# Optimization experiments

Hardware: AMD Instinct MI355X
Metric: run time of the kernel (lower is better)

## Reference

```python
import jax, jax.numpy as jnp
import numpy as np


def setup_inputs() -> dict:
    key = jax.random.key(0)
    k1, k2, k3 = jax.random.split(key, 3)
    B, N, L, H, E = 4, 4, 1024, 8, 64
    queries = jax.random.normal(k1, (B, N, L, H, E), dtype=jnp.float32)
    keys = jax.random.normal(k2, (B, N, L, H, E), dtype=jnp.float32)
    values = jax.random.normal(k3, (B, N, L, H, E), dtype=jnp.float32)
    return {"queries": queries, "keys": keys, "values": values}


def reference(queries, keys, values):
    B, N, L, H, E = queries.shape
    S = values.shape[2]
    scale = 1.0 / jnp.sqrt(jnp.asarray(E, queries.dtype))
    # scores: [B, N, H, L, S]
    scores = jnp.einsum('bnlhe,bnshe->bnhls', queries, keys)
    # causal mask: True above the diagonal (future positions), broadcast over b,n,h
    causal = jnp.triu(jnp.ones((L, S), dtype=bool), k=1)
    scores = jnp.where(causal, -jnp.inf, scores)
    A = jax.nn.softmax(scale * scores, axis=-1)  # dropout p=0.0 -> identity
    V = jnp.einsum('bnhls,bnshd->bnlhd', A, values)
    return V
```

## Files before the change

kernel.cpp:

```cpp
#include <hip/hip_runtime.h>
#include <hip/hip_bf16.h>


typedef __bf16 bf16x8 __attribute__((ext_vector_type(8)));
typedef float  f32x16 __attribute__((ext_vector_type(16)));
typedef unsigned int u32x4 __attribute__((ext_vector_type(4)));

#define SEQ 1024
#define ROWSTRIDE 512
#define LDSPAD 72

__device__ inline bf16x8 pack8(float4 a, float4 b) {
    bf16x8 f;
    f[0]=(__bf16)a.x; f[1]=(__bf16)a.y; f[2]=(__bf16)a.z; f[3]=(__bf16)a.w;
    f[4]=(__bf16)b.x; f[5]=(__bf16)b.y; f[6]=(__bf16)b.z; f[7]=(__bf16)b.w;
    return f;
}
__device__ inline bf16x8 pack8s(float4 a, float4 b, float s) {
    bf16x8 f;
    f[0]=(__bf16)(a.x*s); f[1]=(__bf16)(a.y*s); f[2]=(__bf16)(a.z*s); f[3]=(__bf16)(a.w*s);
    f[4]=(__bf16)(b.x*s); f[5]=(__bf16)(b.y*s); f[6]=(__bf16)(b.z*s); f[7]=(__bf16)(b.w*s);
    return f;
}
__device__ inline unsigned int packbf2(float a, float b) {
    unsigned short ua = __builtin_bit_cast(unsigned short, (__bf16)a);
    unsigned short ub = __builtin_bit_cast(unsigned short, (__bf16)b);
    return (unsigned int)ua | ((unsigned int)ub << 16);
}

__device__ inline void lds_barrier() {
    asm volatile("s_waitcnt lgkmcnt(0)\n\ts_barrier" ::: "memory");
}

__global__ __launch_bounds__(256) void attn_fwd(
    const float* __restrict__ Qg,
    const float* __restrict__ Kg,
    const float* __restrict__ Vg,
    float* __restrict__ Og)
{
    __shared__ __bf16 Kds[64][LDSPAD];
    __shared__ __bf16 Vds[64][LDSPAD];

    const int blk  = blockIdx.x;
    const int t    = blk >> 7;
    const int head = blk & 127;
    const int h_   = head & 7;
    const int bn   = head >> 3;
    const int qt0  = 2 * t, qt1 = 2 * t + 1;

    const int tid  = threadIdx.x;
    const int wave = tid >> 6;
    const int lane = tid & 63;
    const int hh   = lane >> 5;
    const int l31  = lane & 31;
    const int l15  = lane & 15;
    const int state = l31 >> 4;

    const size_t base = (size_t)bn * SEQ * ROWSTRIDE + (size_t)h_ * 64;

    const int qt_lane   = state ? qt1 : qt0;
    const int q_in_tile = wave * 16 + l15;
    const int qrow_lane = qt_lane * 64 + q_in_tile;

    const float kscale = 0.125f * 1.44269504088896f;

    bf16x8 qf[4];
    {
        const float* qp = Qg + base + (size_t)qrow_lane * ROWSTRIDE + 8 * hh;
        #pragma unroll
        for (int ks = 0; ks < 4; ++ks)
            qf[ks] = pack8s(*(const float4*)(qp + 16 * ks),
                            *(const float4*)(qp + 16 * ks + 4), kscale);
    }

    f32x16 o[2];
    #pragma unroll
    for (int et = 0; et < 2; ++et)
        #pragma unroll
        for (int i = 0; i < 16; ++i) o[et][i] = 0.f;
    float lsum = 0.f;

    const int sr = tid >> 2, sc = (tid & 3) << 4;
    const int ve = tid & 63, vs = (tid >> 6) << 4;

    const int ntiles = qt1 + 1;
    const float* kbase = Kg + base;
    const float* vbase = Vg + base;

    float4 kpre[4];
    float  vpre[16];
    {
        const float* kp = kbase + (size_t)sr * ROWSTRIDE + sc;
        #pragma unroll
        for (int i = 0; i < 4; ++i) kpre[i] = *(const float4*)(kp + i * 4);
        const float* vp = vbase + (size_t)vs * ROWSTRIDE + ve;
        #pragma unroll
        for (int j = 0; j < 16; ++j) vpre[j] = vp[(size_t)j * ROWSTRIDE];
    }

    for (int tile = 0; tile < ntiles; ++tile) {
        lds_barrier();

        *(bf16x8*)&Kds[sr][sc]     = pack8(kpre[0], kpre[1]);
        *(bf16x8*)&Kds[sr][sc + 8] = pack8(kpre[2], kpre[3]);
        {
            bf16x8 f0, f1;
            #pragma unroll
            for (int jj = 0; jj < 8; ++jj) { f0[jj] = (__bf16)vpre[jj]; f1[jj] = (__bf16)vpre[8 + jj]; }
            *(bf16x8*)&Vds[ve][vs]     = f0;
            *(bf16x8*)&Vds[ve][vs + 8] = f1;
        }

        if (tile + 1 < ntiles) {
            const int s0n = (tile + 1) * 64;
            const float* kp = kbase + (size_t)(s0n + sr) * ROWSTRIDE + sc;
            #pragma unroll
            for (int i = 0; i < 4; ++i) kpre[i] = *(const float4*)(kp + i * 4);
            const float* vp = vbase + (size_t)(s0n + vs) * ROWSTRIDE + ve;
            #pragma unroll
            for (int j = 0; j < 16; ++j) vpre[j] = vp[(size_t)j * ROWSTRIDE];
        }

        lds_barrier();

        const bool masked = (tile >= qt0);
        const int slimit = !masked ? 64
                         : ((tile < qt_lane) ? 64
                         : ((tile == qt_lane) ? q_in_tile : -1));

        #pragma unroll
        for (int st2 = 0; st2 < 2; ++st2) {
            f32x16 s16;
            #pragma unroll
            for (int i = 0; i < 16; ++i) s16[i] = 0.f;
            #pragma unroll
            for (int ks = 0; ks < 4; ++ks) {
                bf16x8 kb = *(const bf16x8*)&Kds[st2 * 32 + l31][ks * 16 + 8 * hh];
                s16 = __builtin_amdgcn_mfma_f32_32x32x16_bf16(kb, qf[ks], s16, 0, 0, 0);
            }
            unsigned int Dp[8];
            float ps[16];
            if (!masked) {
                #pragma unroll
                for (int reg = 0; reg < 16; ++reg) {
                    float p = __builtin_amdgcn_exp2f(s16[reg]);
                    lsum += p;
                    ps[reg] = p;
                }
            } else {
                #pragma unroll
                for (int reg = 0; reg < 16; ++reg) {
                    const int s_in = st2 * 32 + (reg & 3) + 8 * (reg >> 2) + 4 * hh;
                    float p = (s_in <= slimit) ? __builtin_amdgcn_exp2f(s16[reg]) : 0.f;
                    lsum += p;
                    ps[reg] = p;
                }
            }
            #pragma unroll
            for (int i = 0; i < 8; ++i) Dp[i] = packbf2(ps[2 * i], ps[2 * i + 1]);

            #pragma unroll
            for (int kh = 0; kh < 2; ++kh) {
                const int ks = st2 * 2 + kh;
                const int ka = 4 * kh;
                unsigned int own0 = hh ? Dp[ka + 2] : Dp[ka + 0];
                unsigned int own1 = hh ? Dp[ka + 3] : Dp[ka + 1];
                unsigned int snd0 = hh ? Dp[ka + 0] : Dp[ka + 2];
                unsigned int snd1 = hh ? Dp[ka + 1] : Dp[ka + 3];
                unsigned int x0 = (unsigned int)__shfl_xor((int)snd0, 32);
                unsigned int x1 = (unsigned int)__shfl_xor((int)snd1, 32);
                u32x4 g;
                g[0] = hh ? x0 : own0;
                g[1] = hh ? x1 : own1;
                g[2] = hh ? own0 : x0;
                g[3] = hh ? own1 : x1;
                bf16x8 pf = __builtin_bit_cast(bf16x8, g);
                #pragma unroll
                for (int et = 0; et < 2; ++et) {
                    bf16x8 vb = *(const bf16x8*)&Vds[et * 32 + l31][ks * 16 + 8 * hh];
                    o[et] = __builtin_amdgcn_mfma_f32_32x32x16_bf16(vb, pf, o[et], 0, 0, 0);
                }
            }
        }
    }

    lsum += __shfl_xor(lsum, 32);
    const float inv_l = 1.f / lsum;
    float* op = Og + base + (size_t)qrow_lane * ROWSTRIDE + 4 * hh;
    #pragma unroll
    for (int et = 0; et < 2; ++et) {
        #pragma unroll
        for (int g = 0; g < 4; ++g) {
            float4 v;
            v.x = o[et][4 * g + 0] * inv_l;
            v.y = o[et][4 * g + 1] * inv_l;
            v.z = o[et][4 * g + 2] * inv_l;
            v.w = o[et][4 * g + 3] * inv_l;
            *(float4*)(op + et * 32 + g * 8) = v;
        }
    }
}

extern "C" void kernel_launch(void* const* d_in, const int* in_sizes, int n_in,
                              void* d_out, int out_size, void* d_ws, size_t ws_size,
                              hipStream_t stream) {
    const float* Qg = (const float*)d_in[0];
    const float* Kg = (const float*)d_in[1];
    const float* Vg = (const float*)d_in[2];
    float* Og = (float*)d_out;
    attn_fwd<<<dim3(1024), dim3(256), 0, stream>>>(Qg, Kg, Vg, Og);
}
```

Before: 164.5 us.

## Assign one query tile per two-wave block and skip masked diagonal subblocks

Each 256-thread block used to cover two interleaved 64-row query tiles and run the key loop up to the later tile, so lanes of the earlier tile computed fully masked scores. Now each 128-thread block handles a single query tile, with each wave owning 32 contiguous rows, and runs only as many key tiles as its own causal extent needs. On the diagonal tile, each wave skips the 32x32 subblock that lies fully above the diagonal. The trade-offs: K/V tiles are reused across fewer query rows, so global traffic for K/V rises. Each thread also prefetches twice as many K/V elements, which raises register pressure.

```diff
diff --git a/kernel.cpp b/kernel.cpp
--- a/kernel.cpp
+++ b/kernel.cpp
@@ -32,7 +32,7 @@
     asm volatile("s_waitcnt lgkmcnt(0)\n\ts_barrier" ::: "memory");
 }
 
-__global__ __launch_bounds__(256) void attn_fwd(
+__global__ __launch_bounds__(128, 4) void attn_fwd(
     const float* __restrict__ Qg,
     const float* __restrict__ Kg,
     const float* __restrict__ Vg,
@@ -42,31 +42,27 @@
     __shared__ __bf16 Vds[64][LDSPAD];
 
     const int blk  = blockIdx.x;
-    const int t    = blk >> 7;
+    const int qt   = blk >> 7;
     const int head = blk & 127;
     const int h_   = head & 7;
     const int bn   = head >> 3;
-    const int qt0  = 2 * t, qt1 = 2 * t + 1;
 
     const int tid  = threadIdx.x;
     const int wave = tid >> 6;
     const int lane = tid & 63;
     const int hh   = lane >> 5;
     const int l31  = lane & 31;
-    const int l15  = lane & 15;
-    const int state = l31 >> 4;
 
     const size_t base = (size_t)bn * SEQ * ROWSTRIDE + (size_t)h_ * 64;
 
-    const int qt_lane   = state ? qt1 : qt0;
-    const int q_in_tile = wave * 16 + l15;
-    const int qrow_lane = qt_lane * 64 + q_in_tile;
+    const int q_in_tile = wave * 32 + l31;
+    const int qrow      = qt * 64 + q_in_tile;
 
     const float kscale = 0.125f * 1.44269504088896f;
 
     bf16x8 qf[4];
     {
-        const float* qp = Qg + base + (size_t)qrow_lane * ROWSTRIDE + 8 * hh;
+        const float* qp = Qg + base + (size_t)qrow * ROWSTRIDE + 8 * hh;
         #pragma unroll
         for (int ks = 0; ks < 4; ++ks)
             qf[ks] = pack8s(*(const float4*)(qp + 16 * ks),
@@ -80,56 +76,57 @@
         for (int i = 0; i < 16; ++i) o[et][i] = 0.f;
     float lsum = 0.f;
 
-    const int sr = tid >> 2, sc = (tid & 3) << 4;
-    const int ve = tid & 63, vs = (tid >> 6) << 4;
-
-    const int ntiles = qt1 + 1;
+    const int sr = tid >> 1, sc = (tid & 1) << 5;
+    const int ve = tid & 63, vs0 = (tid >> 6) << 5;
+
+    const int ntiles = qt + 1;
     const float* kbase = Kg + base;
     const float* vbase = Vg + base;
 
-    float4 kpre[4];
-    float  vpre[16];
+    float4 kpre[8];
+    float  vpre[32];
     {
         const float* kp = kbase + (size_t)sr * ROWSTRIDE + sc;
         #pragma unroll
-        for (int i = 0; i < 4; ++i) kpre[i] = *(const float4*)(kp + i * 4);
-        const float* vp = vbase + (size_t)vs * ROWSTRIDE + ve;
-        #pragma unroll
-        for (int j = 0; j < 16; ++j) vpre[j] = vp[(size_t)j * ROWSTRIDE];
+        for (int i = 0; i < 8; ++i) kpre[i] = *(const float4*)(kp + i * 4);
+        const float* vp = vbase + (size_t)vs0 * ROWSTRIDE + ve;
+        #pragma unroll
+        for (int j = 0; j < 32; ++j) vpre[j] = vp[(size_t)j * ROWSTRIDE];
     }
 
     for (int tile = 0; tile < ntiles; ++tile) {
         lds_barrier();
 
-        *(bf16x8*)&Kds[sr][sc]     = pack8(kpre[0], kpre[1]);
-        *(bf16x8*)&Kds[sr][sc + 8] = pack8(kpre[2], kpre[3]);
-        {
-            bf16x8 f0, f1;
-            #pragma unroll
-            for (int jj = 0; jj < 8; ++jj) { f0[jj] = (__bf16)vpre[jj]; f1[jj] = (__bf16)vpre[8 + jj]; }
-            *(bf16x8*)&Vds[ve][vs]     = f0;
-            *(bf16x8*)&Vds[ve][vs + 8] = f1;
+        #pragma unroll
+        for (int w = 0; w < 4; ++w)
+            *(bf16x8*)&Kds[sr][sc + 8 * w] = pack8(kpre[2 * w], kpre[2 * w + 1]);
+        #pragma unroll
+        for (int w = 0; w < 4; ++w) {
+            bf16x8 f;
+            #pragma unroll
+            for (int jj = 0; jj < 8; ++jj) f[jj] = (__bf16)vpre[8 * w + jj];
+            *(bf16x8*)&Vds[ve][vs0 + 8 * w] = f;
         }
 
         if (tile + 1 < ntiles) {
             const int s0n = (tile + 1) * 64;
             const float* kp = kbase + (size_t)(s0n + sr) * ROWSTRIDE + sc;
             #pragma unroll
-            for (int i = 0; i < 4; ++i) kpre[i] = *(const float4*)(kp + i * 4);
-            const float* vp = vbase + (size_t)(s0n + vs) * ROWSTRIDE + ve;
-            #pragma unroll
-            for (int j = 0; j < 16; ++j) vpre[j] = vp[(size_t)j * ROWSTRIDE];
+            for (int i = 0; i < 8; ++i) kpre[i] = *(const float4*)(kp + i * 4);
+            const float* vp = vbase + (size_t)(s0n + vs0) * ROWSTRIDE + ve;
+            #pragma unroll
+            for (int j = 0; j < 32; ++j) vpre[j] = vp[(size_t)j * ROWSTRIDE];
         }
 
         lds_barrier();
 
-        const bool masked = (tile >= qt0);
-        const int slimit = !masked ? 64
-                         : ((tile < qt_lane) ? 64
-                         : ((tile == qt_lane) ? q_in_tile : -1));
+        const bool diagtile = (tile == qt);
 
         #pragma unroll
         for (int st2 = 0; st2 < 2; ++st2) {
+            if (diagtile && st2 > wave) continue;
+            const bool maskon = diagtile && (st2 == wave);
+
             f32x16 s16;
             #pragma unroll
             for (int i = 0; i < 16; ++i) s16[i] = 0.f;
@@ -140,7 +137,7 @@
             }
             unsigned int Dp[8];
             float ps[16];
-            if (!masked) {
+            if (!maskon) {
                 #pragma unroll
                 for (int reg = 0; reg < 16; ++reg) {
                     float p = __builtin_amdgcn_exp2f(s16[reg]);
@@ -150,8 +147,8 @@
             } else {
                 #pragma unroll
                 for (int reg = 0; reg < 16; ++reg) {
-                    const int s_in = st2 * 32 + (reg & 3) + 8 * (reg >> 2) + 4 * hh;
-                    float p = (s_in <= slimit) ? __builtin_amdgcn_exp2f(s16[reg]) : 0.f;
+                    const int roff = (reg & 3) + 8 * (reg >> 2) + 4 * hh;
+                    float p = (roff <= l31) ? __builtin_amdgcn_exp2f(s16[reg]) : 0.f;
                     lsum += p;
                     ps[reg] = p;
                 }
@@ -186,7 +183,7 @@
 
     lsum += __shfl_xor(lsum, 32);
     const float inv_l = 1.f / lsum;
-    float* op = Og + base + (size_t)qrow_lane * ROWSTRIDE + 4 * hh;
+    float* op = Og + base + (size_t)qrow * ROWSTRIDE + 4 * hh;
     #pragma unroll
     for (int et = 0; et < 2; ++et) {
         #pragma unroll
@@ -208,5 +205,5 @@
     const float* Kg = (const float*)d_in[1];
     const float* Vg = (const float*)d_in[2];
     float* Og = (float*)d_out;
-    attn_fwd<<<dim3(1024), dim3(256), 0, stream>>>(Qg, Kg, Vg, Og);
-}
+    attn_fwd<<<dim3(2048), dim3(128), 0, stream>>>(Qg, Kg, Vg, Og);
+}
```

Measured after the change: 278.6 us. 69.4% more time.
